# Kernel optimization log

Measured on AMD Instinct MI355X. Metric: run time of the kernel, lower is better.

Reference implementation:

```python
import jax, jax.numpy as jnp
import numpy as np

LN_EPS = 1e-5


def setup_inputs() -> dict:
    key = jax.random.key(0)
    ks = jax.random.split(key, 10)
    B, N, C, H = 4, 100000, 50000, 64
    E = 300000  # node2class edges (avg arity 3)
    embedding = jax.random.normal(ks[0], (B, N, H), dtype=jnp.float32) / np.sqrt(H).astype(np.float32)
    W1 = jax.random.normal(ks[1], (H, H), dtype=jnp.float32) / np.sqrt(H).astype(np.float32)
    b1 = jax.random.normal(ks[2], (H,), dtype=jnp.float32) * 0.01
    gamma = jnp.ones((H,), dtype=jnp.float32)
    beta = jnp.zeros((H,), dtype=jnp.float32)
    W2 = jax.random.normal(ks[3], (H, 1), dtype=jnp.float32) / np.sqrt(H).astype(np.float32)
    b2 = jnp.zeros((1,), dtype=jnp.float32)
    n2c_row = jax.random.randint(ks[4], (E,), 0, N, dtype=jnp.int32)
    n2c_col = jax.random.randint(ks[5], (E,), 0, C, dtype=jnp.int32)
    c2n_row = jax.random.randint(ks[6], (N,), 0, C, dtype=jnp.int32)
    c2n_col = jnp.arange(N, dtype=jnp.int32)
    return {
        "embedding": embedding, "W1": W1, "b1": b1, "gamma": gamma, "beta": beta,
        "W2": W2, "b2": b2,
        "n2c_row": n2c_row, "n2c_col": n2c_col,
        "c2n_row": c2n_row, "c2n_col": c2n_col,
        "num_classes": C,
    }


def _seg_mean(data, seg_ids, num_segments):
    # data: [E, H], seg_ids: [E] -> [num_segments, H] mean-aggregation
    s = jax.ops.segment_sum(data, seg_ids, num_segments=num_segments)
    cnt = jax.ops.segment_sum(jnp.ones_like(seg_ids, dtype=data.dtype), seg_ids,
                              num_segments=num_segments)
    return s / jnp.maximum(cnt, 1.0)[:, None]


def reference(embedding, W1, b1, gamma, beta, W2, b2,
              n2c_row, n2c_col, c2n_row, c2n_col, num_classes):
    B, N, H = embedding.shape
    # class2node mean aggregation: eclass embedding = mean of member enode embeddings
    class_emb = jax.vmap(lambda e: _seg_mean(e[c2n_col], c2n_row, num_classes))(embedding)  # [B,C,H]
    # node2class mean aggregation: enode context = mean over child eclass embeddings
    node_ctx = jax.vmap(lambda c: _seg_mean(c[n2c_col], n2c_row, N))(class_emb)  # [B,N,H]
    x = embedding + node_ctx
    # enode_proj -> LayerNorm -> ReLU -> Dropout(p=0) -> output_proj (forward_embedding)
    h = jnp.einsum('bnh,hk->bnk', x, W1) + b1
    mu = jnp.mean(h, axis=-1, keepdims=True)
    var = jnp.mean(jnp.square(h - mu), axis=-1, keepdims=True)
    h = (h - mu) * jax.lax.rsqrt(var + LN_EPS) * gamma + beta
    h = jax.nn.relu(h)
    logit = jnp.einsum('bnh,ho->bno', h, W2)[..., 0] + b2[0]  # [B, N]
    return logit
```

## Files before the change

kernel.cpp:

```cpp
#include <hip/hip_runtime.h>
#include <cstddef>

#define HH 64

struct WS {
  int* scanb;
  int* cur;
  int* part;
  int* melist;
  float* cmean;
};

__device__ __forceinline__ WS ws_layout(void* d_ws, int C, int N, int E) {
  int* wi = (int*)d_ws;
  WS w;
  w.scanb  = wi;
  w.cur    = wi + (size_t)(C + N);
  w.part   = w.cur + (size_t)(C + N);
  w.melist = w.part + 1024;
  size_t fo = (size_t)2 * (C + N) + 1024 + (size_t)(N + E);
  fo = (fo + 3) & ~(size_t)3;
  w.cmean = (float*)d_ws + fo;
  return w;
}

__global__ __launch_bounds__(256) void k_init(void* ws, const int* __restrict__ pC,
                                              int N, int E) {
  int C = *pC;
  WS w = ws_layout(ws, C, N, E);
  size_t total = (size_t)2 * (C + N);
  size_t stride = (size_t)gridDim.x * blockDim.x;
  for (size_t i = (size_t)blockIdx.x * blockDim.x + threadIdx.x; i < total; i += stride)
    w.scanb[i] = 0;
}

__global__ __launch_bounds__(256) void k_count(const int* __restrict__ c2n_row,
                                               const int* __restrict__ n2c_row,
                                               void* ws, const int* __restrict__ pC,
                                               int N, int E) {
  int C = *pC;
  WS w = ws_layout(ws, C, N, E);
  int idx = blockIdx.x * 256 + threadIdx.x;
  if (idx < N) {
    atomicAdd(&w.scanb[c2n_row[idx]], 1);
  } else if (idx < N + E) {
    atomicAdd(&w.scanb[C + n2c_row[idx - N]], 1);
  }
}

__global__ __launch_bounds__(256) void k_scan_blk(void* ws, const int* __restrict__ pC,
                                                  int N, int E) {
  int C = *pC;
  WS w = ws_layout(ws, C, N, E);
  int L = C + N;
  __shared__ int tmp[256];
  int gid = blockIdx.x * 256 + threadIdx.x;
  int v = (gid < L) ? w.scanb[gid] : 0;
  tmp[threadIdx.x] = v;
  __syncthreads();
#pragma unroll
  for (int off = 1; off < 256; off <<= 1) {
    int t = (threadIdx.x >= (unsigned)off) ? tmp[threadIdx.x - off] : 0;
    __syncthreads();
    tmp[threadIdx.x] += t;
    __syncthreads();
  }
  if (gid < L) w.scanb[gid] = tmp[threadIdx.x] - v;
  if (threadIdx.x == 255) w.part[blockIdx.x] = tmp[255];
}

__global__ __launch_bounds__(1024) void k_scan_part(void* ws, const int* __restrict__ pC,
                                                    int N, int E) {
  int C = *pC;
  WS w = ws_layout(ws, C, N, E);
  __shared__ int tmp[1024];
  int v = w.part[threadIdx.x];
  tmp[threadIdx.x] = v;
  __syncthreads();
#pragma unroll
  for (int off = 1; off < 1024; off <<= 1) {
    int t = (threadIdx.x >= (unsigned)off) ? tmp[threadIdx.x - off] : 0;
    __syncthreads();
    tmp[threadIdx.x] += t;
    __syncthreads();
  }
  w.part[threadIdx.x] = tmp[threadIdx.x] - v;
}

__global__ __launch_bounds__(256) void k_scan_add(void* ws, const int* __restrict__ pC,
                                                  int N, int E) {
  int C = *pC;
  WS w = ws_layout(ws, C, N, E);
  int L = C + N;
  int gid = blockIdx.x * 256 + threadIdx.x;
  if (gid < L) w.scanb[gid] += w.part[blockIdx.x];
}

__global__ __launch_bounds__(256) void k_fill(const int* __restrict__ c2n_row,
                                              const int* __restrict__ n2c_row,
                                              const int* __restrict__ n2c_col,
                                              void* ws, const int* __restrict__ pC,
                                              int N, int E) {
  int C = *pC;
  WS w = ws_layout(ws, C, N, E);
  int idx = blockIdx.x * 256 + threadIdx.x;
  if (idx < N) {
    int c = c2n_row[idx];
    int pos = w.scanb[c] + atomicAdd(&w.cur[c], 1);
    w.melist[pos] = idx;
  } else if (idx < N + E) {
    int e = idx - N;
    int nn = n2c_row[e];
    int pos = w.scanb[C + nn] + atomicAdd(&w.cur[C + nn], 1);
    w.melist[pos] = n2c_col[e];
  }
}

__global__ __launch_bounds__(256) void k_class_mean(const float* __restrict__ emb,
                                                    void* ws, const int* __restrict__ pC,
                                                    int N, int E, int B) {
  int C = *pC;
  WS w = ws_layout(ws, C, N, E);
  int lane = threadIdx.x & 63;
  int wav = (int)((blockIdx.x * (size_t)blockDim.x + threadIdx.x) >> 6);
  int nw = (int)(((size_t)gridDim.x * blockDim.x) >> 6);
  size_t NH = (size_t)N * HH;
  size_t CH = (size_t)C * HH;
  for (int c = wav; c < C; c += nw) {
    int start = w.scanb[c];
    int deg = w.cur[c];
    float inv = 1.0f / fmaxf((float)deg, 1.0f);
    if (B == 4) {
      float s0 = 0, s1 = 0, s2 = 0, s3 = 0;
      for (int k = 0; k < deg; ++k) {
        int m = w.melist[start + k];
        size_t base = (size_t)m * HH + lane;
        s0 += emb[base];
        s1 += emb[base + NH];
        s2 += emb[base + 2 * NH];
        s3 += emb[base + 3 * NH];
      }
      size_t o = (size_t)c * HH + lane;
      w.cmean[o] = s0 * inv;
      w.cmean[o + CH] = s1 * inv;
      w.cmean[o + 2 * CH] = s2 * inv;
      w.cmean[o + 3 * CH] = s3 * inv;
    } else {
      for (int b = 0; b < B; ++b) {
        float s = 0;
        for (int k = 0; k < deg; ++k) {
          int m = w.melist[start + k];
          s += emb[((size_t)b * N + m) * HH + lane];
        }
        w.cmean[((size_t)b * C + c) * HH + lane] = s * inv;
      }
    }
  }
}

__global__ __launch_bounds__(256) void k_mlp(
    const float* __restrict__ emb, const float* __restrict__ W1,
    const float* __restrict__ b1, const float* __restrict__ gamma,
    const float* __restrict__ beta, const float* __restrict__ W2,
    const float* __restrict__ b2, void* ws, const int* __restrict__ pC,
    float* __restrict__ out, int N, int E) {
  __shared__ float w1s[HH * HH];
  for (int t = threadIdx.x; t < HH * HH / 4; t += blockDim.x)
    ((float4*)w1s)[t] = ((const float4*)W1)[t];
  __syncthreads();

  int C = *pC;
  WS w = ws_layout(ws, C, N, E);

  int b = blockIdx.y;
  int n = blockIdx.x * 256 + threadIdx.x;
  if (n >= N) return;
  size_t rowoff = ((size_t)b * N + n) * HH;

  float x[HH];
  const float4* e4 = (const float4*)(emb + rowoff);
#pragma unroll
  for (int q = 0; q < HH / 4; ++q) {
    float4 ev = e4[q];
    x[4 * q + 0] = ev.x;
    x[4 * q + 1] = ev.y;
    x[4 * q + 2] = ev.z;
    x[4 * q + 3] = ev.w;
  }

  int start = w.scanb[C + n];
  int deg = w.cur[C + n];
  if (deg > 0) {
    float inv = 1.0f / (float)deg;
    for (int k = 0; k < deg; ++k) {
      int col = w.melist[start + k];
      const float4* c4 = (const float4*)(w.cmean + ((size_t)b * C + col) * HH);
#pragma unroll
      for (int q = 0; q < HH / 4; ++q) {
        float4 cv = c4[q];
        x[4 * q + 0] += inv * cv.x;
        x[4 * q + 1] += inv * cv.y;
        x[4 * q + 2] += inv * cv.z;
        x[4 * q + 3] += inv * cv.w;
      }
    }
  }

  float h[HH];
#pragma unroll
  for (int q = 0; q < HH / 4; ++q) {
    float4 bv = *(const float4*)(b1 + 4 * q);
    h[4 * q + 0] = bv.x;
    h[4 * q + 1] = bv.y;
    h[4 * q + 2] = bv.z;
    h[4 * q + 3] = bv.w;
  }
#pragma unroll
  for (int i = 0; i < HH; ++i) {
    float xi = x[i];
#pragma unroll
    for (int q = 0; q < HH / 4; ++q) {
      float4 wv = *(const float4*)(w1s + i * HH + 4 * q);
      h[4 * q + 0] += xi * wv.x;
      h[4 * q + 1] += xi * wv.y;
      h[4 * q + 2] += xi * wv.z;
      h[4 * q + 3] += xi * wv.w;
    }
  }

  float mu = 0.0f;
#pragma unroll
  for (int j = 0; j < HH; ++j) mu += h[j];
  mu *= (1.0f / HH);
  float var = 0.0f;
#pragma unroll
  for (int j = 0; j < HH; ++j) {
    float d = h[j] - mu;
    var += d * d;
  }
  var *= (1.0f / HH);
  float rs = rsqrtf(var + 1e-5f);

  float logit = b2[0];
#pragma unroll
  for (int j = 0; j < HH; ++j) {
    float hn = (h[j] - mu) * rs * gamma[j] + beta[j];
    hn = fmaxf(hn, 0.0f);
    logit += hn * W2[j];
  }
  out[(size_t)b * N + n] = logit;
}

extern "C" void kernel_launch(void* const* d_in, const int* in_sizes, int n_in,
                              void* d_out, int out_size, void* d_ws,
                              size_t ws_size, hipStream_t stream) {
  const float* emb   = (const float*)d_in[0];
  const float* W1    = (const float*)d_in[1];
  const float* b1    = (const float*)d_in[2];
  const float* gamma = (const float*)d_in[3];
  const float* beta  = (const float*)d_in[4];
  const float* W2    = (const float*)d_in[5];
  const float* b2    = (const float*)d_in[6];
  const int* n2c_row = (const int*)d_in[7];
  const int* n2c_col = (const int*)d_in[8];
  const int* c2n_row = (const int*)d_in[9];
  const int* pC      = (const int*)d_in[11];

  int E = in_sizes[7];
  int N = in_sizes[9];
  int H = in_sizes[2];
  int B = in_sizes[0] / (N * H);
  (void)n_in; (void)ws_size; (void)out_size;

  float* out = (float*)d_out;

  int ne_blocks = (N + E + 255) / 256;

  k_init<<<1024, 256, 0, stream>>>(d_ws, pC, N, E);
  k_count<<<ne_blocks, 256, 0, stream>>>(c2n_row, n2c_row, d_ws, pC, N, E);
  k_scan_blk<<<1024, 256, 0, stream>>>(d_ws, pC, N, E);
  k_scan_part<<<1, 1024, 0, stream>>>(d_ws, pC, N, E);
  k_scan_add<<<1024, 256, 0, stream>>>(d_ws, pC, N, E);
  k_fill<<<ne_blocks, 256, 0, stream>>>(c2n_row, n2c_row, n2c_col, d_ws, pC, N, E);

  k_class_mean<<<2048, 256, 0, stream>>>(emb, d_ws, pC, N, E, B);

  dim3 gm((unsigned)((N + 255) / 256), (unsigned)B);
  k_mlp<<<gm, 256, 0, stream>>>(emb, W1, b1, gamma, beta, W2, b2, d_ws, pC, out,
                                N, E);
}
```

Before: 350.8 us.

## Pre-project class means through W1 and fold scan offsets into consumers

Uses linearity to compute G = cmean·W1 once per class in a new kernel, so the MLP kernel multiplies only the node embedding by W1 and accumulates the projected class rows. This trades a per-node 64x64 matvec on the aggregated input for a per-class matvec over fewer rows plus an extra B*C*H buffer write and read. The separate scan-add kernel is removed by adding the block partial sums at each lookup. The class-mean grid is also doubled.

```diff
diff --git a/kernel.cpp b/kernel.cpp
--- a/kernel.cpp
+++ b/kernel.cpp
@@ -9,9 +9,10 @@
   int* part;
   int* melist;
   float* cmean;
+  float* g;
 };
 
-__device__ __forceinline__ WS ws_layout(void* d_ws, int C, int N, int E) {
+__device__ __forceinline__ WS ws_layout(void* d_ws, int C, int N, int E, int B) {
   int* wi = (int*)d_ws;
   WS w;
   w.scanb  = wi;
@@ -21,13 +22,14 @@
   size_t fo = (size_t)2 * (C + N) + 1024 + (size_t)(N + E);
   fo = (fo + 3) & ~(size_t)3;
   w.cmean = (float*)d_ws + fo;
+  w.g     = w.cmean + (size_t)B * C * HH;
   return w;
 }
 
 __global__ __launch_bounds__(256) void k_init(void* ws, const int* __restrict__ pC,
-                                              int N, int E) {
-  int C = *pC;
-  WS w = ws_layout(ws, C, N, E);
+                                              int N, int E, int B) {
+  int C = *pC;
+  WS w = ws_layout(ws, C, N, E, B);
   size_t total = (size_t)2 * (C + N);
   size_t stride = (size_t)gridDim.x * blockDim.x;
   for (size_t i = (size_t)blockIdx.x * blockDim.x + threadIdx.x; i < total; i += stride)
@@ -37,9 +39,9 @@
 __global__ __launch_bounds__(256) void k_count(const int* __restrict__ c2n_row,
                                                const int* __restrict__ n2c_row,
                                                void* ws, const int* __restrict__ pC,
-                                               int N, int E) {
-  int C = *pC;
-  WS w = ws_layout(ws, C, N, E);
+                                               int N, int E, int B) {
+  int C = *pC;
+  WS w = ws_layout(ws, C, N, E, B);
   int idx = blockIdx.x * 256 + threadIdx.x;
   if (idx < N) {
     atomicAdd(&w.scanb[c2n_row[idx]], 1);
@@ -49,9 +51,9 @@
 }
 
 __global__ __launch_bounds__(256) void k_scan_blk(void* ws, const int* __restrict__ pC,
-                                                  int N, int E) {
-  int C = *pC;
-  WS w = ws_layout(ws, C, N, E);
+                                                  int N, int E, int B) {
+  int C = *pC;
+  WS w = ws_layout(ws, C, N, E, B);
   int L = C + N;
   __shared__ int tmp[256];
   int gid = blockIdx.x * 256 + threadIdx.x;
@@ -70,9 +72,9 @@
 }
 
 __global__ __launch_bounds__(1024) void k_scan_part(void* ws, const int* __restrict__ pC,
-                                                    int N, int E) {
-  int C = *pC;
-  WS w = ws_layout(ws, C, N, E);
+                                                    int N, int E, int B) {
+  int C = *pC;
+  WS w = ws_layout(ws, C, N, E, B);
   __shared__ int tmp[1024];
   int v = w.part[threadIdx.x];
   tmp[threadIdx.x] = v;
@@ -87,31 +89,22 @@
   w.part[threadIdx.x] = tmp[threadIdx.x] - v;
 }
 
-__global__ __launch_bounds__(256) void k_scan_add(void* ws, const int* __restrict__ pC,
-                                                  int N, int E) {
-  int C = *pC;
-  WS w = ws_layout(ws, C, N, E);
-  int L = C + N;
-  int gid = blockIdx.x * 256 + threadIdx.x;
-  if (gid < L) w.scanb[gid] += w.part[blockIdx.x];
-}
-
 __global__ __launch_bounds__(256) void k_fill(const int* __restrict__ c2n_row,
                                               const int* __restrict__ n2c_row,
                                               const int* __restrict__ n2c_col,
                                               void* ws, const int* __restrict__ pC,
-                                              int N, int E) {
-  int C = *pC;
-  WS w = ws_layout(ws, C, N, E);
+                                              int N, int E, int B) {
+  int C = *pC;
+  WS w = ws_layout(ws, C, N, E, B);
   int idx = blockIdx.x * 256 + threadIdx.x;
   if (idx < N) {
     int c = c2n_row[idx];
-    int pos = w.scanb[c] + atomicAdd(&w.cur[c], 1);
+    int pos = w.scanb[c] + w.part[c >> 8] + atomicAdd(&w.cur[c], 1);
     w.melist[pos] = idx;
   } else if (idx < N + E) {
     int e = idx - N;
-    int nn = n2c_row[e];
-    int pos = w.scanb[C + nn] + atomicAdd(&w.cur[C + nn], 1);
+    int seg = C + n2c_row[e];
+    int pos = w.scanb[seg] + w.part[seg >> 8] + atomicAdd(&w.cur[seg], 1);
     w.melist[pos] = n2c_col[e];
   }
 }
@@ -120,14 +113,14 @@
                                                     void* ws, const int* __restrict__ pC,
                                                     int N, int E, int B) {
   int C = *pC;
-  WS w = ws_layout(ws, C, N, E);
+  WS w = ws_layout(ws, C, N, E, B);
   int lane = threadIdx.x & 63;
   int wav = (int)((blockIdx.x * (size_t)blockDim.x + threadIdx.x) >> 6);
   int nw = (int)(((size_t)gridDim.x * blockDim.x) >> 6);
   size_t NH = (size_t)N * HH;
   size_t CH = (size_t)C * HH;
   for (int c = wav; c < C; c += nw) {
-    int start = w.scanb[c];
+    int start = w.scanb[c] + w.part[c >> 8];
     int deg = w.cur[c];
     float inv = 1.0f / fmaxf((float)deg, 1.0f);
     if (B == 4) {
@@ -158,53 +151,64 @@
   }
 }
 
+__global__ __launch_bounds__(256) void k_g(const float* __restrict__ W1, void* ws,
+                                           const int* __restrict__ pC,
+                                           int N, int E, int B) {
+  __shared__ float w1s[HH * HH];
+  for (int t = threadIdx.x; t < HH * HH / 4; t += 256)
+    ((float4*)w1s)[t] = ((const float4*)W1)[t];
+  __syncthreads();
+
+  int C = *pC;
+  WS w = ws_layout(ws, C, N, E, B);
+  size_t total = (size_t)B * C;
+  size_t stride = (size_t)gridDim.x * 256;
+  for (size_t r = (size_t)blockIdx.x * 256 + threadIdx.x; r < total; r += stride) {
+    const float4* src = (const float4*)(w.cmean + r * HH);
+    float h[HH];
+#pragma unroll
+    for (int k = 0; k < HH; ++k) h[k] = 0.0f;
+#pragma unroll
+    for (int q = 0; q < HH / 4; ++q) {
+      float4 cv = src[q];
+#pragma unroll
+      for (int j = 0; j < 4; ++j) {
+        float ci = (j == 0) ? cv.x : (j == 1) ? cv.y : (j == 2) ? cv.z : cv.w;
+        const float4* wrow = (const float4*)(w1s + (4 * q + j) * HH);
+#pragma unroll
+        for (int kq = 0; kq < HH / 4; ++kq) {
+          float4 wv = wrow[kq];
+          h[4 * kq + 0] += ci * wv.x;
+          h[4 * kq + 1] += ci * wv.y;
+          h[4 * kq + 2] += ci * wv.z;
+          h[4 * kq + 3] += ci * wv.w;
+        }
+      }
+    }
+    float4* dst = (float4*)(w.g + r * HH);
+#pragma unroll
+    for (int kq = 0; kq < HH / 4; ++kq)
+      dst[kq] = make_float4(h[4 * kq], h[4 * kq + 1], h[4 * kq + 2], h[4 * kq + 3]);
+  }
+}
+
 __global__ __launch_bounds__(256) void k_mlp(
     const float* __restrict__ emb, const float* __restrict__ W1,
     const float* __restrict__ b1, const float* __restrict__ gamma,
     const float* __restrict__ beta, const float* __restrict__ W2,
     const float* __restrict__ b2, void* ws, const int* __restrict__ pC,
-    float* __restrict__ out, int N, int E) {
+    float* __restrict__ out, int N, int E, int B) {
   __shared__ float w1s[HH * HH];
-  for (int t = threadIdx.x; t < HH * HH / 4; t += blockDim.x)
+  for (int t = threadIdx.x; t < HH * HH / 4; t += 256)
     ((float4*)w1s)[t] = ((const float4*)W1)[t];
   __syncthreads();
 
   int C = *pC;
-  WS w = ws_layout(ws, C, N, E);
+  WS w = ws_layout(ws, C, N, E, B);
 
   int b = blockIdx.y;
   int n = blockIdx.x * 256 + threadIdx.x;
   if (n >= N) return;
-  size_t rowoff = ((size_t)b * N + n) * HH;
-
-  float x[HH];
-  const float4* e4 = (const float4*)(emb + rowoff);
-#pragma unroll
-  for (int q = 0; q < HH / 4; ++q) {
-    float4 ev = e4[q];
-    x[4 * q + 0] = ev.x;
-    x[4 * q + 1] = ev.y;
-    x[4 * q + 2] = ev.z;
-    x[4 * q + 3] = ev.w;
-  }
-
-  int start = w.scanb[C + n];
-  int deg = w.cur[C + n];
-  if (deg > 0) {
-    float inv = 1.0f / (float)deg;
-    for (int k = 0; k < deg; ++k) {
-      int col = w.melist[start + k];
-      const float4* c4 = (const float4*)(w.cmean + ((size_t)b * C + col) * HH);
-#pragma unroll
-      for (int q = 0; q < HH / 4; ++q) {
-        float4 cv = c4[q];
-        x[4 * q + 0] += inv * cv.x;
-        x[4 * q + 1] += inv * cv.y;
-        x[4 * q + 2] += inv * cv.z;
-        x[4 * q + 3] += inv * cv.w;
-      }
-    }
-  }
 
   float h[HH];
 #pragma unroll
@@ -215,16 +219,42 @@
     h[4 * q + 2] = bv.z;
     h[4 * q + 3] = bv.w;
   }
-#pragma unroll
-  for (int i = 0; i < HH; ++i) {
-    float xi = x[i];
-#pragma unroll
-    for (int q = 0; q < HH / 4; ++q) {
-      float4 wv = *(const float4*)(w1s + i * HH + 4 * q);
-      h[4 * q + 0] += xi * wv.x;
-      h[4 * q + 1] += xi * wv.y;
-      h[4 * q + 2] += xi * wv.z;
-      h[4 * q + 3] += xi * wv.w;
+
+  const float4* e4 = (const float4*)(emb + ((size_t)b * N + n) * HH);
+#pragma unroll
+  for (int q = 0; q < HH / 4; ++q) {
+    float4 ev = e4[q];
+#pragma unroll
+    for (int j = 0; j < 4; ++j) {
+      float xi = (j == 0) ? ev.x : (j == 1) ? ev.y : (j == 2) ? ev.z : ev.w;
+      const float4* wrow = (const float4*)(w1s + (4 * q + j) * HH);
+#pragma unroll
+      for (int kq = 0; kq < HH / 4; ++kq) {
+        float4 wv = wrow[kq];
+        h[4 * kq + 0] += xi * wv.x;
+        h[4 * kq + 1] += xi * wv.y;
+        h[4 * kq + 2] += xi * wv.z;
+        h[4 * kq + 3] += xi * wv.w;
+      }
+    }
+  }
+
+  int seg = C + n;
+  int start = w.scanb[seg] + w.part[seg >> 8];
+  int deg = w.cur[seg];
+  if (deg > 0) {
+    float inv = 1.0f / (float)deg;
+    for (int k = 0; k < deg; ++k) {
+      int col = w.melist[start + k];
+      const float4* g4 = (const float4*)(w.g + ((size_t)b * C + col) * HH);
+#pragma unroll
+      for (int q = 0; q < HH / 4; ++q) {
+        float4 gv = g4[q];
+        h[4 * q + 0] += inv * gv.x;
+        h[4 * q + 1] += inv * gv.y;
+        h[4 * q + 2] += inv * gv.z;
+        h[4 * q + 3] += inv * gv.w;
+      }
     }
   }
 
@@ -276,16 +306,16 @@
 
   int ne_blocks = (N + E + 255) / 256;
 
-  k_init<<<1024, 256, 0, stream>>>(d_ws, pC, N, E);
-  k_count<<<ne_blocks, 256, 0, stream>>>(c2n_row, n2c_row, d_ws, pC, N, E);
-  k_scan_blk<<<1024, 256, 0, stream>>>(d_ws, pC, N, E);
-  k_scan_part<<<1, 1024, 0, stream>>>(d_ws, pC, N, E);
-  k_scan_add<<<1024, 256, 0, stream>>>(d_ws, pC, N, E);
-  k_fill<<<ne_blocks, 256, 0, stream>>>(c2n_row, n2c_row, n2c_col, d_ws, pC, N, E);
-
-  k_class_mean<<<2048, 256, 0, stream>>>(emb, d_ws, pC, N, E, B);
+  k_init<<<1024, 256, 0, stream>>>(d_ws, pC, N, E, B);
+  k_count<<<ne_blocks, 256, 0, stream>>>(c2n_row, n2c_row, d_ws, pC, N, E, B);
+  k_scan_blk<<<1024, 256, 0, stream>>>(d_ws, pC, N, E, B);
+  k_scan_part<<<1, 1024, 0, stream>>>(d_ws, pC, N, E, B);
+  k_fill<<<ne_blocks, 256, 0, stream>>>(c2n_row, n2c_row, n2c_col, d_ws, pC, N, E, B);
+
+  k_class_mean<<<4096, 256, 0, stream>>>(emb, d_ws, pC, N, E, B);
+  k_g<<<2048, 256, 0, stream>>>(W1, d_ws, pC, N, E, B);
 
   dim3 gm((unsigned)((N + 255) / 256), (unsigned)B);
   k_mlp<<<gm, 256, 0, stream>>>(emb, W1, b1, gamma, beta, W2, b2, d_ws, pC, out,
-                                N, E);
-}
+                                N, E, B);
+}
```

Measured after the change: 557.8 us. +59.0%, slower.
